# Performance work log

Measured on AMD Instinct MI355X. Metric: run time of the kernel, lower is better.

## Reference

```python
import jax, jax.numpy as jnp
import numpy as np

D, H, HS, L, V, B, T = 384, 8, 48, 8, 32000, 32, 128
EPS = 1e-5


def setup_inputs() -> dict:
    key = jax.random.key(0)
    ks = jax.random.split(key, 10)
    s = 0.02
    return {
        'index': jax.random.randint(ks[0], (B, T), 0, V),
        'tok_emb': jax.random.normal(ks[1], (V, D), jnp.float32) * s,
        'pos_emb': jax.random.normal(ks[2], (V, D), jnp.float32) * s,
        'Wq': jax.random.normal(ks[3], (L, D, D), jnp.float32) * s,
        'Wk': jax.random.normal(ks[4], (L, D, D), jnp.float32) * s,
        'Wv': jax.random.normal(ks[5], (L, D, D), jnp.float32) * s,
        'Wo': jax.random.normal(ks[6], (L, D, D), jnp.float32) * s,
        'bo': jnp.zeros((L, D), jnp.float32),
        'W1': jax.random.normal(ks[7], (L, D, 4 * D), jnp.float32) * s,
        'b1': jnp.zeros((L, 4 * D), jnp.float32),
        'W2': jax.random.normal(ks[8], (L, 4 * D, D), jnp.float32) * s,
        'b2': jnp.zeros((L, D), jnp.float32),
        'ln1g': jnp.ones((L, D), jnp.float32),
        'ln1b': jnp.zeros((L, D), jnp.float32),
        'ln2g': jnp.ones((L, D), jnp.float32),
        'ln2b': jnp.zeros((L, D), jnp.float32),
        'lnfg': jnp.ones((D,), jnp.float32),
        'lnfb': jnp.zeros((D,), jnp.float32),
        'lmW': jax.random.normal(ks[9], (D, V), jnp.float32) * s,
        'lmb': jnp.zeros((V,), jnp.float32),
    }


def _layer_norm(x, g, b):
    m = jnp.mean(x, axis=-1, keepdims=True)
    xc = x - m
    v = jnp.mean(xc * xc, axis=-1, keepdims=True)
    return xc * jax.lax.rsqrt(v + EPS) * g + b


def _forward(index, tok_emb, pos_emb, Wq, Wk, Wv, Wo, bo, W1, b1, W2, b2,
             ln1g, ln1b, ln2g, ln2b, lnfg, lnfb, lmW, lmb):
    Bx, Tx = index.shape
    x = tok_emb[index] + pos_emb[jnp.arange(Tx)]  # [B,T,D]
    tril = jnp.tril(jnp.ones((Tx, Tx), bool))
    scale = HS ** -0.5
    neg_inf = jnp.finfo(x.dtype).min
    for l in range(L):
        q = (x @ Wq[l]).reshape(Bx, Tx, H, HS)
        k = (x @ Wk[l]).reshape(Bx, Tx, H, HS)
        v = (x @ Wv[l]).reshape(Bx, Tx, H, HS)
        wei = jnp.einsum('bthd,bshd->bhts', q, k) * scale  # [B,H,T,T]
        wei = jnp.where(tril, wei, neg_inf)
        wei = jax.nn.softmax(wei, axis=-1)
        attn = jnp.einsum('bhts,bshd->bthd', wei, v).reshape(Bx, Tx, D)
        y = attn @ Wo[l] + bo[l]
        x = _layer_norm(x + y, ln1g[l], ln1b[l])  # post-LN as in source
        y = jax.nn.relu(x @ W1[l] + b1[l]) @ W2[l] + b2[l]
        x = _layer_norm(x + y, ln2g[l], ln2b[l])
    x = _layer_norm(x, lnfg, lnfb)
    logits = x @ lmW + lmb  # [B,T,V]
    return logits


def reference(index, tok_emb, pos_emb, Wq, Wk, Wv, Wo, bo, W1, b1, W2, b2,
              ln1g, ln1b, ln2g, ln2b, lnfg, lnfb, lmW, lmb):
    return _forward(index, tok_emb, pos_emb, Wq, Wk, Wv, Wo, bo, W1, b1, W2,
                    b2, ln1g, ln1b, ln2g, ln2b, lnfg, lnfb, lmW, lmb)
```

## Files before the change

kernel.cpp:

```cpp
#include <hip/hip_runtime.h>
#include <cstdint>
#include <cstddef>

#define D_  384
#define H_  8
#define HS_ 48
#define L_  8
#define V_  32000
#define B_  32
#define T_  128
#define M_  4096

typedef __bf16 bf16;
typedef __bf16 bf16x8 __attribute__((ext_vector_type(8)));
typedef float  floatx4 __attribute__((ext_vector_type(4)));

__device__ __forceinline__ unsigned short bfbits(float f) {
  union { bf16 b; unsigned short u; } cv; cv.b = (bf16)f; return cv.u;
}

__device__ __forceinline__ float waveReduceSum(float v) {
  #pragma unroll
  for (int off = 32; off > 0; off >>= 1) v += __shfl_xor(v, off, 64);
  return v;
}

__global__ void embed_kernel(const int* __restrict__ idx, const float* __restrict__ tok,
                             const float* __restrict__ pos, float* __restrict__ x,
                             bf16* __restrict__ xb) {
  int e = blockIdx.x * 256 + threadIdx.x;
  int row = e / 96, c4 = (e % 96) * 4;
  int t = row & (T_ - 1);
  int tk = idx[row];
  const float4 tv = *(const float4*)(tok + (size_t)tk * D_ + c4);
  const float4 pv = *(const float4*)(pos + (size_t)t * D_ + c4);
  float4 o; o.x = tv.x + pv.x; o.y = tv.y + pv.y; o.z = tv.z + pv.z; o.w = tv.w + pv.w;
  *(float4*)(x + (size_t)row * D_ + c4) = o;
  uint2 u;
  u.x = (unsigned)bfbits(o.x) | ((unsigned)bfbits(o.y) << 16);
  u.y = (unsigned)bfbits(o.z) | ((unsigned)bfbits(o.w) << 16);
  *(uint2*)(xb + (size_t)row * D_ + c4) = u;
}

__device__ __forceinline__ void transpose_tile(const float* __restrict__ src, bf16* __restrict__ dst,
                                               int K, int N, int k0, int n0) {
  __shared__ float tile[32][33];
  const int r = threadIdx.x >> 5, c = threadIdx.x & 31;
  #pragma unroll
  for (int i = 0; i < 4; i++)
    tile[r + 8*i][c] = src[(size_t)(k0 + r + 8*i) * N + n0 + c];
  __syncthreads();
  #pragma unroll
  for (int i = 0; i < 4; i++)
    dst[(size_t)(n0 + r + 8*i) * K + k0 + c] = (bf16)tile[c][r + 8*i];
}

__global__ void t_qkvo_kernel(const float* __restrict__ Wq, const float* __restrict__ Wk,
                              const float* __restrict__ Wv, const float* __restrict__ Wo,
                              bf16* __restrict__ dst) {
  const float* src = blockIdx.z == 0 ? Wq : blockIdx.z == 1 ? Wk : blockIdx.z == 2 ? Wv : Wo;
  transpose_tile(src, dst + (size_t)blockIdx.z * (D_ * D_), D_, D_, blockIdx.y * 32, blockIdx.x * 32);
}

__global__ void t_ffn_kernel(const float* __restrict__ W1, const float* __restrict__ W2,
                             bf16* __restrict__ w1t, bf16* __restrict__ w2t) {
  if (blockIdx.z == 0) {
    if (blockIdx.x >= 48 || blockIdx.y >= 12) return;
    transpose_tile(W1, w1t, D_, 4 * D_, blockIdx.y * 32, blockIdx.x * 32);
  } else {
    if (blockIdx.x >= 12 || blockIdx.y >= 48) return;
    transpose_tile(W2, w2t, 4 * D_, D_, blockIdx.y * 32, blockIdx.x * 32);
  }
}

__global__ void t_head_kernel(const float* __restrict__ lmW, bf16* __restrict__ dst) {
  transpose_tile(lmW, dst, D_, V_, blockIdx.y * 32, blockIdx.x * 32);
}

template<bool BIAS, bool RESID, bool RELU, bool OUTBF>
__device__ __forceinline__ void gemm_core(
    const bf16* __restrict__ A, const bf16* __restrict__ Bt,
    const float* __restrict__ bias, const float* __restrict__ resid,
    void* __restrict__ Cout, int N, int K, int m0, int n0)
{
  __shared__ bf16 As[128][56];
  __shared__ bf16 Bs[128][56];
  const int tid  = threadIdx.x;
  const int lane = tid & 63;
  const int wave = tid >> 6;
  const int wr = wave >> 1, wc = wave & 1;
  const int lrow = lane & 15, quad = lane >> 4;

  floatx4 acc[4][4];
  #pragma unroll
  for (int i = 0; i < 4; i++)
    #pragma unroll
    for (int j = 0; j < 4; j++) acc[i][j] = floatx4{0.f, 0.f, 0.f, 0.f};

  const int r0 = tid >> 2,          p0 = (tid & 3) * 8;
  const int r1 = (tid + 256) >> 2,  p1 = p0;

  for (int k0 = 0; k0 < K; k0 += 32) {
    __syncthreads();
    const uint4 a0 = *(const uint4*)(A  + (size_t)(m0 + r0) * K + k0 + p0);
    const uint4 a1 = *(const uint4*)(A  + (size_t)(m0 + r1) * K + k0 + p1);
    const uint4 b0 = *(const uint4*)(Bt + (size_t)(n0 + r0) * K + k0 + p0);
    const uint4 b1 = *(const uint4*)(Bt + (size_t)(n0 + r1) * K + k0 + p1);
    *(uint4*)&As[r0][p0] = a0;
    *(uint4*)&As[r1][p1] = a1;
    *(uint4*)&Bs[r0][p0] = b0;
    *(uint4*)&Bs[r1][p1] = b1;
    __syncthreads();
    bf16x8 af[4], bfr[4];
    #pragma unroll
    for (int mt = 0; mt < 4; mt++) af[mt]  = *(const bf16x8*)&As[wr*64 + mt*16 + lrow][quad*8];
    #pragma unroll
    for (int nt = 0; nt < 4; nt++) bfr[nt] = *(const bf16x8*)&Bs[wc*64 + nt*16 + lrow][quad*8];
    #pragma unroll
    for (int mt = 0; mt < 4; mt++)
      #pragma unroll
      for (int nt = 0; nt < 4; nt++)
        acc[mt][nt] = __builtin_amdgcn_mfma_f32_16x16x32_bf16(af[mt], bfr[nt], acc[mt][nt], 0, 0, 0);
  }

  #pragma unroll
  for (int mt = 0; mt < 4; mt++) {
    #pragma unroll
    for (int nt = 0; nt < 4; nt++) {
      const int col = n0 + wc*64 + nt*16 + lrow;
      float bv = 0.f;
      if (BIAS) bv = bias[col];
      #pragma unroll
      for (int i = 0; i < 4; i++) {
        const int row = m0 + wr*64 + mt*16 + quad*4 + i;
        float vv = acc[mt][nt][i] + bv;
        if (RESID) vv += resid[(size_t)row * N + col];
        if (RELU)  vv = vv > 0.f ? vv : 0.f;
        if (OUTBF) ((bf16*)Cout)[(size_t)row * N + col] = (bf16)vv;
        else       ((float*)Cout)[(size_t)row * N + col] = vv;
      }
    }
  }
}

template<bool BIAS, bool RESID, bool RELU, bool OUTBF>
__global__ __launch_bounds__(256) void gemm_kernel(const bf16* __restrict__ A, const bf16* __restrict__ Bt,
    const float* __restrict__ bias, const float* __restrict__ resid, void* __restrict__ C, int N, int K) {
  gemm_core<BIAS, RESID, RELU, OUTBF>(A, Bt, bias, resid, C, N, K, blockIdx.x * 128, blockIdx.y * 128);
}

__global__ __launch_bounds__(256) void gemm_qkv_kernel(const bf16* __restrict__ A, const bf16* __restrict__ Wt,
    float* __restrict__ q, float* __restrict__ k, float* __restrict__ v) {
  const bf16* Bt = Wt + (size_t)blockIdx.z * (D_ * D_);
  float* C = blockIdx.z == 0 ? q : (blockIdx.z == 1 ? k : v);
  gemm_core<false, false, false, false>(A, Bt, nullptr, nullptr, C, D_, D_, blockIdx.x * 128, blockIdx.y * 128);
}

__global__ __launch_bounds__(128) void attn_kernel(const float* __restrict__ q,
    const float* __restrict__ k, const float* __restrict__ v, bf16* __restrict__ attnb) {
  __shared__ float ks[T_][52];
  __shared__ float vs[T_][52];
  const int bh = blockIdx.x;
  const int b = bh >> 3, h = bh & 7;
  const int r = threadIdx.x;
  const size_t rowbase = ((size_t)(b * T_ + r)) * D_ + h * HS_;
  #pragma unroll
  for (int j = 0; j < 12; j++) {
    *(float4*)&ks[r][4*j] = *(const float4*)(k + rowbase + 4*j);
    *(float4*)&vs[r][4*j] = *(const float4*)(v + rowbase + 4*j);
  }
  float qr[48];
  #pragma unroll
  for (int j = 0; j < 12; j++) {
    const float4 t = *(const float4*)(q + rowbase + 4*j);
    qr[4*j] = t.x; qr[4*j+1] = t.y; qr[4*j+2] = t.z; qr[4*j+3] = t.w;
  }
  __syncthreads();
  float m = -3.0e38f, l = 0.f, acc[48];
  #pragma unroll
  for (int j = 0; j < 48; j++) acc[j] = 0.f;
  const float scale = 0.14433756729740643f;
  for (int c = 0; c < T_; c++) {
    float s0 = 0.f, s1 = 0.f, s2 = 0.f, s3 = 0.f;
    #pragma unroll
    for (int j = 0; j < 48; j += 4) {
      s0 += qr[j]   * ks[c][j];
      s1 += qr[j+1] * ks[c][j+1];
      s2 += qr[j+2] * ks[c][j+2];
      s3 += qr[j+3] * ks[c][j+3];
    }
    float s = ((s0 + s1) + (s2 + s3)) * scale;
    if (c > r) s = -3.0e38f;
    const float mn = fmaxf(m, s);
    const float al = __expf(m - mn);
    const float pp = __expf(s - mn);
    l = l * al + pp;
    #pragma unroll
    for (int j = 0; j < 48; j++) acc[j] = acc[j] * al + pp * vs[c][j];
    m = mn;
  }
  const float inv = 1.f / l;
  unsigned ob[24];
  #pragma unroll
  for (int j = 0; j < 24; j++)
    ob[j] = (unsigned)bfbits(acc[2*j] * inv) | ((unsigned)bfbits(acc[2*j+1] * inv) << 16);
  bf16* dst = attnb + rowbase;
  #pragma unroll
  for (int j = 0; j < 6; j++) {
    uint4 u; u.x = ob[4*j]; u.y = ob[4*j+1]; u.z = ob[4*j+2]; u.w = ob[4*j+3];
    *(uint4*)(dst + 8*j) = u;
  }
}

__global__ __launch_bounds__(256) void ln_kernel(const float* __restrict__ in,
    const float* __restrict__ g, const float* __restrict__ bta,
    float* __restrict__ xo, bf16* __restrict__ xbo) {
  const int wave = threadIdx.x >> 6, lane = threadIdx.x & 63;
  const int row = blockIdx.x * 4 + wave;
  const float* p = in + (size_t)row * D_;
  float v[6];
  #pragma unroll
  for (int j = 0; j < 6; j++) v[j] = p[lane + 64*j];
  float s = 0.f;
  #pragma unroll
  for (int j = 0; j < 6; j++) s += v[j];
  s = waveReduceSum(s);
  const float mean = s * (1.f / 384.f);
  float qv = 0.f;
  #pragma unroll
  for (int j = 0; j < 6; j++) { v[j] -= mean; qv += v[j] * v[j]; }
  qv = waveReduceSum(qv);
  const float rs = rsqrtf(qv * (1.f / 384.f) + 1e-5f);
  #pragma unroll
  for (int j = 0; j < 6; j++) {
    const int c = lane + 64*j;
    const float o = v[j] * rs * g[c] + bta[c];
    xo[(size_t)row * D_ + c]  = o;
    xbo[(size_t)row * D_ + c] = (bf16)o;
  }
}

extern "C" void kernel_launch(void* const* d_in, const int* in_sizes, int n_in,
                              void* d_out, int out_size, void* d_ws, size_t ws_size,
                              hipStream_t stream) {
  const int*   index = (const int*)  d_in[0];
  const float* tok   = (const float*)d_in[1];
  const float* pos   = (const float*)d_in[2];
  const float* Wq    = (const float*)d_in[3];
  const float* Wk    = (const float*)d_in[4];
  const float* Wv    = (const float*)d_in[5];
  const float* Wo    = (const float*)d_in[6];
  const float* bo    = (const float*)d_in[7];
  const float* W1    = (const float*)d_in[8];
  const float* b1    = (const float*)d_in[9];
  const float* W2    = (const float*)d_in[10];
  const float* b2    = (const float*)d_in[11];
  const float* ln1g  = (const float*)d_in[12];
  const float* ln1b  = (const float*)d_in[13];
  const float* ln2g  = (const float*)d_in[14];
  const float* ln2b  = (const float*)d_in[15];
  const float* lnfg  = (const float*)d_in[16];
  const float* lnfb  = (const float*)d_in[17];
  const float* lmW   = (const float*)d_in[18];
  const float* lmb   = (const float*)d_in[19];
  float* out = (float*)d_out;
  char* ws = (char*)d_ws;

  float* x     = (float*)(ws + 0);
  float* tmp   = (float*)(ws + 6291456);
  bf16*  xb    = (bf16*) (ws + 12582912);
  float* qbuf  = (float*)(ws + 15728640);
  float* kbuf  = (float*)(ws + 22020096);
  float* vbuf  = (float*)(ws + 28311552);
  bf16*  attnb = (bf16*) (ws + 34603008);
  bf16*  hb    = (bf16*) (ws + 37748736);
  bf16* wqkvoT = (bf16*)(ws + 37748736);
  bf16* w1t    = (bf16*)(ws + 34603008);
  bf16* w2t    = (bf16*)(ws + 34603008 + 1179648);
  bf16* lmT    = (bf16*)(ws + 15728640);

  embed_kernel<<<1536, 256, 0, stream>>>(index, tok, pos, x, xb);
  for (int l = 0; l < L_; l++) {
    t_qkvo_kernel<<<dim3(12, 12, 4), 256, 0, stream>>>(
        Wq + (size_t)l * D_ * D_, Wk + (size_t)l * D_ * D_,
        Wv + (size_t)l * D_ * D_, Wo + (size_t)l * D_ * D_, wqkvoT);
    gemm_qkv_kernel<<<dim3(32, 3, 3), 256, 0, stream>>>(xb, wqkvoT, qbuf, kbuf, vbuf);
    attn_kernel<<<256, 128, 0, stream>>>(qbuf, kbuf, vbuf, attnb);
    gemm_kernel<true, true, false, false><<<dim3(32, 3), 256, 0, stream>>>(
        attnb, wqkvoT + 3 * D_ * D_, bo + l * D_, x, tmp, D_, D_);
    ln_kernel<<<1024, 256, 0, stream>>>(tmp, ln1g + l * D_, ln1b + l * D_, x, xb);
    t_ffn_kernel<<<dim3(48, 48, 2), 256, 0, stream>>>(
        W1 + (size_t)l * D_ * 4 * D_, W2 + (size_t)l * 4 * D_ * D_, w1t, w2t);
    gemm_kernel<true, false, true, true><<<dim3(32, 12), 256, 0, stream>>>(
        xb, w1t, b1 + l * 4 * D_, nullptr, hb, 4 * D_, D_);
    gemm_kernel<true, true, false, false><<<dim3(32, 3), 256, 0, stream>>>(
        hb, w2t, b2 + l * D_, x, tmp, D_, 4 * D_);
    ln_kernel<<<1024, 256, 0, stream>>>(tmp, ln2g + l * D_, ln2b + l * D_, x, xb);
  }
  ln_kernel<<<1024, 256, 0, stream>>>(x, lnfg, lnfb, x, xb);
  t_head_kernel<<<dim3(1000, 12), 256, 0, stream>>>(lmW, lmT);
  gemm_kernel<true, false, false, false><<<dim3(32, 250), 256, 0, stream>>>(
      xb, lmT, lmb, nullptr, out, V_, D_);
}
```

Baseline: 2.033 ms.

## Split attention head dim across 4 threads, bf16 QKV, merge weight transposes

Attention now assigns four threads per query row, each handling 12 of the 48 head dims. Partial dot products are combined with wave shuffles, and the block grows to 512 threads. This raises the thread count from 128 per block and cuts per-thread register arrays, which should improve occupancy in the layer's main latency-bound kernel. The QKV GEMM now writes bf16 instead of fp32, halving that traffic, and the per-layer weight transposes are merged into one launch with a rearranged workspace layout. The cost is bf16 rounding of q/k/v and extra shuffle work.

```diff
diff --git a/kernel.cpp b/kernel.cpp
--- a/kernel.cpp
+++ b/kernel.cpp
@@ -17,6 +17,12 @@
 
 __device__ __forceinline__ unsigned short bfbits(float f) {
   union { bf16 b; unsigned short u; } cv; cv.b = (bf16)f; return cv.u;
+}
+__device__ __forceinline__ float bflo(unsigned u) {
+  union { float f; unsigned x; } c; c.x = u << 16; return c.f;
+}
+__device__ __forceinline__ float bfhi(unsigned u) {
+  union { float f; unsigned x; } c; c.x = u & 0xffff0000u; return c.f;
 }
 
 __device__ __forceinline__ float waveReduceSum(float v) {
@@ -55,25 +61,23 @@
     dst[(size_t)(n0 + r + 8*i) * K + k0 + c] = (bf16)tile[c][r + 8*i];
 }
 
-__global__ void t_qkvo_kernel(const float* __restrict__ Wq, const float* __restrict__ Wk,
-                              const float* __restrict__ Wv, const float* __restrict__ Wo,
-                              bf16* __restrict__ dst) {
-  const float* src = blockIdx.z == 0 ? Wq : blockIdx.z == 1 ? Wk : blockIdx.z == 2 ? Wv : Wo;
-  transpose_tile(src, dst + (size_t)blockIdx.z * (D_ * D_), D_, D_, blockIdx.y * 32, blockIdx.x * 32);
-}
-
-__global__ void t_ffn_kernel(const float* __restrict__ W1, const float* __restrict__ W2,
-                             bf16* __restrict__ w1t, bf16* __restrict__ w2t) {
+__global__ __launch_bounds__(256) void t_layer_kernel(
+    const float* __restrict__ Wq, const float* __restrict__ Wk,
+    const float* __restrict__ Wv, const float* __restrict__ Wo,
+    const float* __restrict__ W1, const float* __restrict__ W2,
+    bf16* __restrict__ wqkvoT, bf16* __restrict__ w1t, bf16* __restrict__ w2t) {
   if (blockIdx.z == 0) {
-    if (blockIdx.x >= 48 || blockIdx.y >= 12) return;
+    const int mm = blockIdx.x / 12, nx = blockIdx.x % 12;
+    const float* src = mm == 0 ? Wq : mm == 1 ? Wk : mm == 2 ? Wv : Wo;
+    transpose_tile(src, wqkvoT + (size_t)mm * (D_ * D_), D_, D_, blockIdx.y * 32, nx * 32);
+  } else if (blockIdx.z == 1) {
     transpose_tile(W1, w1t, D_, 4 * D_, blockIdx.y * 32, blockIdx.x * 32);
   } else {
-    if (blockIdx.x >= 12 || blockIdx.y >= 48) return;
-    transpose_tile(W2, w2t, 4 * D_, D_, blockIdx.y * 32, blockIdx.x * 32);
-  }
-}
-
-__global__ void t_head_kernel(const float* __restrict__ lmW, bf16* __restrict__ dst) {
+    transpose_tile(W2, w2t, 4 * D_, D_, blockIdx.x * 32, blockIdx.y * 32);
+  }
+}
+
+__global__ __launch_bounds__(256) void t_head_kernel(const float* __restrict__ lmW, bf16* __restrict__ dst) {
   transpose_tile(lmW, dst, D_, V_, blockIdx.y * 32, blockIdx.x * 32);
 }
 
@@ -150,65 +154,67 @@
 }
 
 __global__ __launch_bounds__(256) void gemm_qkv_kernel(const bf16* __restrict__ A, const bf16* __restrict__ Wt,
-    float* __restrict__ q, float* __restrict__ k, float* __restrict__ v) {
+    bf16* __restrict__ q, bf16* __restrict__ k, bf16* __restrict__ v) {
   const bf16* Bt = Wt + (size_t)blockIdx.z * (D_ * D_);
-  float* C = blockIdx.z == 0 ? q : (blockIdx.z == 1 ? k : v);
-  gemm_core<false, false, false, false>(A, Bt, nullptr, nullptr, C, D_, D_, blockIdx.x * 128, blockIdx.y * 128);
-}
-
-__global__ __launch_bounds__(128) void attn_kernel(const float* __restrict__ q,
-    const float* __restrict__ k, const float* __restrict__ v, bf16* __restrict__ attnb) {
-  __shared__ float ks[T_][52];
-  __shared__ float vs[T_][52];
+  bf16* C = blockIdx.z == 0 ? q : (blockIdx.z == 1 ? k : v);
+  gemm_core<false, false, false, true>(A, Bt, nullptr, nullptr, C, D_, D_, blockIdx.x * 128, blockIdx.y * 128);
+}
+
+__global__ __launch_bounds__(512) void attn_kernel(const bf16* __restrict__ q,
+    const bf16* __restrict__ k, const bf16* __restrict__ v, bf16* __restrict__ attnb) {
+  __shared__ float ks[T_][48];
+  __shared__ float vs[T_][48];
   const int bh = blockIdx.x;
   const int b = bh >> 3, h = bh & 7;
-  const int r = threadIdx.x;
-  const size_t rowbase = ((size_t)(b * T_ + r)) * D_ + h * HS_;
-  #pragma unroll
-  for (int j = 0; j < 12; j++) {
-    *(float4*)&ks[r][4*j] = *(const float4*)(k + rowbase + 4*j);
-    *(float4*)&vs[r][4*j] = *(const float4*)(v + rowbase + 4*j);
-  }
-  float qr[48];
-  #pragma unroll
-  for (int j = 0; j < 12; j++) {
-    const float4 t = *(const float4*)(q + rowbase + 4*j);
-    qr[4*j] = t.x; qr[4*j+1] = t.y; qr[4*j+2] = t.z; qr[4*j+3] = t.w;
+  const int r  = threadIdx.x >> 2;
+  const int qq = threadIdx.x & 3;
+  const int o  = qq * 12;
+  const size_t rowbase = ((size_t)(b * T_ + r)) * D_ + h * HS_ + o;
+  float qr[12];
+  #pragma unroll
+  for (int j = 0; j < 3; j++) {
+    const uint2 tk = *(const uint2*)(k + rowbase + 4*j);
+    const uint2 tv = *(const uint2*)(v + rowbase + 4*j);
+    const uint2 tq = *(const uint2*)(q + rowbase + 4*j);
+    float4 fk, fv;
+    fk.x = bflo(tk.x); fk.y = bfhi(tk.x); fk.z = bflo(tk.y); fk.w = bfhi(tk.y);
+    fv.x = bflo(tv.x); fv.y = bfhi(tv.x); fv.z = bflo(tv.y); fv.w = bfhi(tv.y);
+    *(float4*)&ks[r][o + 4*j] = fk;
+    *(float4*)&vs[r][o + 4*j] = fv;
+    qr[4*j]   = bflo(tq.x); qr[4*j+1] = bfhi(tq.x);
+    qr[4*j+2] = bflo(tq.y); qr[4*j+3] = bfhi(tq.y);
   }
   __syncthreads();
-  float m = -3.0e38f, l = 0.f, acc[48];
-  #pragma unroll
-  for (int j = 0; j < 48; j++) acc[j] = 0.f;
+  float m = -3.0e38f, l = 0.f, acc[12];
+  #pragma unroll
+  for (int j = 0; j < 12; j++) acc[j] = 0.f;
   const float scale = 0.14433756729740643f;
   for (int c = 0; c < T_; c++) {
-    float s0 = 0.f, s1 = 0.f, s2 = 0.f, s3 = 0.f;
-    #pragma unroll
-    for (int j = 0; j < 48; j += 4) {
-      s0 += qr[j]   * ks[c][j];
-      s1 += qr[j+1] * ks[c][j+1];
-      s2 += qr[j+2] * ks[c][j+2];
-      s3 += qr[j+3] * ks[c][j+3];
-    }
-    float s = ((s0 + s1) + (s2 + s3)) * scale;
+    float s = 0.f;
+    #pragma unroll
+    for (int j = 0; j < 12; j++) s += qr[j] * ks[c][o + j];
+    s += __shfl_xor(s, 1, 64);
+    s += __shfl_xor(s, 2, 64);
+    s *= scale;
     if (c > r) s = -3.0e38f;
     const float mn = fmaxf(m, s);
     const float al = __expf(m - mn);
     const float pp = __expf(s - mn);
     l = l * al + pp;
     #pragma unroll
-    for (int j = 0; j < 48; j++) acc[j] = acc[j] * al + pp * vs[c][j];
+    for (int j = 0; j < 12; j++) acc[j] = acc[j] * al + pp * vs[c][o + j];
     m = mn;
   }
   const float inv = 1.f / l;
-  unsigned ob[24];
-  #pragma unroll
-  for (int j = 0; j < 24; j++)
+  unsigned ob[6];
+  #pragma unroll
+  for (int j = 0; j < 6; j++)
     ob[j] = (unsigned)bfbits(acc[2*j] * inv) | ((unsigned)bfbits(acc[2*j+1] * inv) << 16);
   bf16* dst = attnb + rowbase;
   #pragma unroll
-  for (int j = 0; j < 6; j++) {
-    uint4 u; u.x = ob[4*j]; u.y = ob[4*j+1]; u.z = ob[4*j+2]; u.w = ob[4*j+3];
-    *(uint4*)(dst + 8*j) = u;
+  for (int j = 0; j < 3; j++) {
+    uint2 u; u.x = ob[2*j]; u.y = ob[2*j+1];
+    *(uint2*)(dst + 4*j) = u;
   }
 }
 
@@ -269,28 +275,28 @@
   float* x     = (float*)(ws + 0);
   float* tmp   = (float*)(ws + 6291456);
   bf16*  xb    = (bf16*) (ws + 12582912);
-  float* qbuf  = (float*)(ws + 15728640);
-  float* kbuf  = (float*)(ws + 22020096);
-  float* vbuf  = (float*)(ws + 28311552);
-  bf16*  attnb = (bf16*) (ws + 34603008);
-  bf16*  hb    = (bf16*) (ws + 37748736);
-  bf16* wqkvoT = (bf16*)(ws + 37748736);
-  bf16* w1t    = (bf16*)(ws + 34603008);
-  bf16* w2t    = (bf16*)(ws + 34603008 + 1179648);
-  bf16* lmT    = (bf16*)(ws + 15728640);
+  bf16*  qb    = (bf16*) (ws + 15728640);
+  bf16*  kb    = (bf16*) (ws + 18874368);
+  bf16*  vb    = (bf16*) (ws + 22020096);
+  bf16*  attnb = (bf16*) (ws + 25165824);
+  bf16*  hb    = (bf16*) (ws + 28311552);
+  bf16*  wqkvoT= (bf16*) (ws + 40894464);
+  bf16*  w1t   = (bf16*) (ws + 42074112);
+  bf16*  w2t   = (bf16*) (ws + 43253760);
+  bf16*  lmT   = (bf16*) (ws + 15728640);
 
   embed_kernel<<<1536, 256, 0, stream>>>(index, tok, pos, x, xb);
   for (int l = 0; l < L_; l++) {
-    t_qkvo_kernel<<<dim3(12, 12, 4), 256, 0, stream>>>(
+    t_layer_kernel<<<dim3(48, 12, 3), 256, 0, stream>>>(
         Wq + (size_t)l * D_ * D_, Wk + (size_t)l * D_ * D_,
-        Wv + (size_t)l * D_ * D_, Wo + (size_t)l * D_ * D_, wqkvoT);
-    gemm_qkv_kernel<<<dim3(32, 3, 3), 256, 0, stream>>>(xb, wqkvoT, qbuf, kbuf, vbuf);
-    attn_kernel<<<256, 128, 0, stream>>>(qbuf, kbuf, vbuf, attnb);
+        Wv + (size_t)l * D_ * D_, Wo + (size_t)l * D_ * D_,
+        W1 + (size_t)l * D_ * 4 * D_, W2 + (size_t)l * 4 * D_ * D_,
+        wqkvoT, w1t, w2t);
+    gemm_qkv_kernel<<<dim3(32, 3, 3), 256, 0, stream>>>(xb, wqkvoT, qb, kb, vb);
+    attn_kernel<<<256, 512, 0, stream>>>(qb, kb, vb, attnb);
     gemm_kernel<true, true, false, false><<<dim3(32, 3), 256, 0, stream>>>(
         attnb, wqkvoT + 3 * D_ * D_, bo + l * D_, x, tmp, D_, D_);
     ln_kernel<<<1024, 256, 0, stream>>>(tmp, ln1g + l * D_, ln1b + l * D_, x, xb);
-    t_ffn_kernel<<<dim3(48, 48, 2), 256, 0, stream>>>(
-        W1 + (size_t)l * D_ * 4 * D_, W2 + (size_t)l * 4 * D_ * D_, w1t, w2t);
     gemm_kernel<true, false, true, true><<<dim3(32, 12), 256, 0, stream>>>(
         xb, w1t, b1 + l * 4 * D_, nullptr, hb, 4 * D_, D_);
     gemm_kernel<true, true, false, false><<<dim3(32, 3), 256, 0, stream>>>(
```

Measured after the change: 1.799 ms. -11.5%, faster.
